# Kernel optimization log

Measured on AMD Instinct MI355X. Metric: run time of the kernel, lower is better.

Reference implementation:

```python
import jax, jax.numpy as jnp
import numpy as np

EPS = 1e-5

def _layer_norm(x, g, b):
    mu = jnp.mean(x, axis=-1, keepdims=True)
    var = jnp.var(x, axis=-1, keepdims=True)
    return (x - mu) * jax.lax.rsqrt(var + EPS) * g + b

def setup_inputs() -> dict:
    key = jax.random.key(0)
    ks = jax.random.split(key, 20)
    B, S, D, L = 64, 1024, 16, 2
    s = 1.0 / np.sqrt(D)
    s2 = 1.0 / np.sqrt(L)
    return {
        "x": jax.random.normal(ks[0], (B, S, D), jnp.float32),
        "Wq": jax.random.uniform(ks[1], (D, L), jnp.float32, -s, s),
        "bq": jax.random.uniform(ks[2], (L,), jnp.float32, -s, s),
        "Wk": jax.random.uniform(ks[3], (D, L), jnp.float32, -s, s),
        "bk": jax.random.uniform(ks[4], (L,), jnp.float32, -s, s),
        "Wv": jax.random.uniform(ks[5], (D, L), jnp.float32, -s, s),
        "bv": jax.random.uniform(ks[6], (L,), jnp.float32, -s, s),
        "Wu": jax.random.uniform(ks[7], (L, D), jnp.float32, -s2, s2),
        "bu": jax.random.uniform(ks[8], (D,), jnp.float32, -s2, s2),
        "ln_g": jnp.ones((D,), jnp.float32),
        "ln_b": jnp.zeros((D,), jnp.float32),
        "W1": jax.random.uniform(ks[9], (D, D), jnp.float32, -s, s),
        "b1": jax.random.uniform(ks[10], (D,), jnp.float32, -s, s),
        "W2": jax.random.uniform(ks[11], (D, D), jnp.float32, -s, s),
        "b2": jax.random.uniform(ks[12], (D,), jnp.float32, -s, s),
        "W3": jax.random.uniform(ks[13], (D, D), jnp.float32, -s, s),
        "b3": jax.random.uniform(ks[14], (D,), jnp.float32, -s, s),
        "Wo": jax.random.uniform(ks[15], (D, D), jnp.float32, -s, s),
        "bo": jax.random.uniform(ks[16], (D,), jnp.float32, -s, s),
    }

def reference(x, Wq, bq, Wk, bk, Wv, bv, Wu, bu, ln_g, ln_b, W1, b1, W2, b2, W3, b3, Wo, bo):
    D = 16  # embedding_dim used as softmax scale in the original
    Q = x @ Wq + bq                      # [B,S,2]
    K = x @ Wk + bk
    V = x @ Wv + bv
    scores = jnp.einsum('bsl,btl->bst', Q, K) / jnp.sqrt(jnp.float32(D))  # [B,S,S]
    attn = jax.nn.softmax(scores, axis=-1)
    ctx = jnp.einsum('bst,btl->bsl', attn, V)  # [B,S,2]
    ctx = ctx @ Wu + bu                         # [B,S,16]
    h = _layer_norm(ctx + x, ln_g, ln_b)
    ff = ((h @ W1 + b1) @ W2 + b2) @ W3 + b3   # 3 linears, no nonlinearity (as in source)
    out = _layer_norm(ff + h, ln_g, ln_b)       # NOTE: same LayerNorm params reused, per source
    return out @ Wo + bo
```

## Files before the change

### kernel.cpp

```cpp
#include <hip/hip_runtime.h>
#include <math.h>


__device__ __forceinline__ void load_row16(const float* __restrict__ p, float* dst) {
    const float4* p4 = (const float4*)p;
    float4 r0 = p4[0], r1 = p4[1], r2 = p4[2], r3 = p4[3];
    dst[0]=r0.x;  dst[1]=r0.y;  dst[2]=r0.z;  dst[3]=r0.w;
    dst[4]=r1.x;  dst[5]=r1.y;  dst[6]=r1.z;  dst[7]=r1.w;
    dst[8]=r2.x;  dst[9]=r2.y;  dst[10]=r2.z; dst[11]=r2.w;
    dst[12]=r3.x; dst[13]=r3.y; dst[14]=r3.z; dst[15]=r3.w;
}

__device__ __forceinline__ void matvec16(const float* v, const float* W,
                                         const float* __restrict__ bias, float* y) {
#pragma unroll
    for (int j = 0; j < 16; ++j) y[j] = bias[j];
#pragma unroll
    for (int i = 0; i < 16; ++i) {
        float vi = v[i];
#pragma unroll
        for (int j = 0; j < 16; ++j) y[j] = fmaf(vi, W[i*16 + j], y[j]);
    }
}

__device__ __forceinline__ void layernorm16(float* h, const float* __restrict__ g,
                                            const float* __restrict__ bb) {
    float mu = 0.f;
#pragma unroll
    for (int j = 0; j < 16; ++j) mu += h[j];
    mu *= 0.0625f;
    float var = 0.f;
#pragma unroll
    for (int j = 0; j < 16; ++j) { float d = h[j] - mu; var = fmaf(d, d, var); }
    var *= 0.0625f;
    float rs = rsqrtf(var + 1e-5f);
#pragma unroll
    for (int j = 0; j < 16; ++j) h[j] = (h[j] - mu) * rs * g[j] + bb[j];
}

__global__ __launch_bounds__(1024)
void fused_encoder(const float* __restrict__ x,
                   const float* __restrict__ Wq, const float* __restrict__ bq,
                   const float* __restrict__ Wk, const float* __restrict__ bk,
                   const float* __restrict__ Wv, const float* __restrict__ bv,
                   const float* __restrict__ Wu, const float* __restrict__ bu,
                   const float* __restrict__ ln_g, const float* __restrict__ ln_b,
                   const float* __restrict__ W1, const float* __restrict__ b1,
                   const float* __restrict__ W2, const float* __restrict__ b2,
                   const float* __restrict__ W3, const float* __restrict__ b3,
                   const float* __restrict__ Wo, const float* __restrict__ bo,
                   float* __restrict__ out)
{
    constexpr int S = 1024, D = 16;

    __shared__ float4 skv[1024];
    __shared__ float4 sred[3][256];
    __shared__ float  sW[4][256];

    const int tid     = threadIdx.x;
    const int b       = blockIdx.x >> 2;
    const int chunk   = blockIdx.x & 3;
    const int q_local = tid & 255;
    const int kslice  = tid >> 8;

    const float* xb = x + (size_t)b * S * D;

    {
        float xr[16];
        load_row16(xb + tid * D, xr);
        float k0 = bk[0], k1 = bk[1], v0 = bv[0], v1 = bv[1];
#pragma unroll
        for (int i = 0; i < 16; ++i) {
            k0 = fmaf(xr[i], Wk[2*i],   k0);
            k1 = fmaf(xr[i], Wk[2*i+1], k1);
            v0 = fmaf(xr[i], Wv[2*i],   v0);
            v1 = fmaf(xr[i], Wv[2*i+1], v1);
        }
        skv[tid] = make_float4(k0, k1, v0, v1);
    }

    {
        const float* Wsel = (kslice == 0) ? W1 : (kslice == 1) ? W2
                          : (kslice == 2) ? W3 : Wo;
        sW[kslice][q_local] = Wsel[q_local];
    }

    const int qi = chunk * 256 + q_local;
    float xq[16];
    load_row16(xb + qi * D, xq);
    float q0 = bq[0], q1 = bq[1];
#pragma unroll
    for (int i = 0; i < 16; ++i) {
        q0 = fmaf(xq[i], Wq[2*i],   q0);
        q1 = fmaf(xq[i], Wq[2*i+1], q1);
    }
    q0 *= 0.25f; q1 *= 0.25f;

    __syncthreads();

    float l0=0.f, l1=0.f, l2=0.f, l3=0.f;
    float a00=0.f, a01=0.f, a02=0.f, a03=0.f;
    float a10=0.f, a11=0.f, a12=0.f, a13=0.f;
    const int t0 = kslice * 256;
    for (int t = 0; t < 256; t += 4) {
        float4 c0 = skv[t0 + t + 0];
        float4 c1 = skv[t0 + t + 1];
        float4 c2 = skv[t0 + t + 2];
        float4 c3 = skv[t0 + t + 3];
        float p0 = __expf(fmaf(q1, c0.y, q0 * c0.x));
        float p1 = __expf(fmaf(q1, c1.y, q0 * c1.x));
        float p2 = __expf(fmaf(q1, c2.y, q0 * c2.x));
        float p3 = __expf(fmaf(q1, c3.y, q0 * c3.x));
        l0 += p0; a00 = fmaf(p0, c0.z, a00); a10 = fmaf(p0, c0.w, a10);
        l1 += p1; a01 = fmaf(p1, c1.z, a01); a11 = fmaf(p1, c1.w, a11);
        l2 += p2; a02 = fmaf(p2, c2.z, a02); a12 = fmaf(p2, c2.w, a12);
        l3 += p3; a03 = fmaf(p3, c3.z, a03); a13 = fmaf(p3, c3.w, a13);
    }
    float l  = (l0 + l1) + (l2 + l3);
    float a0 = (a00 + a01) + (a02 + a03);
    float a1 = (a10 + a11) + (a12 + a13);

    if (kslice > 0) sred[kslice - 1][q_local] = make_float4(l, a0, a1, 0.f);
    __syncthreads();

    if (tid < 256) {
#pragma unroll
        for (int s = 0; s < 3; ++s) {
            float4 r = sred[s][tid];
            l += r.x; a0 += r.y; a1 += r.z;
        }
        float rl = 1.0f / l;
        float c0 = a0 * rl, c1 = a1 * rl;

        float h[16];
#pragma unroll
        for (int j = 0; j < 16; ++j)
            h[j] = fmaf(c0, Wu[j], fmaf(c1, Wu[16 + j], bu[j])) + xq[j];

        layernorm16(h, ln_g, ln_b);

        float t1[16], t2[16], t3[16];
        matvec16(h,  &sW[0][0], b1, t1);
        matvec16(t1, &sW[1][0], b2, t2);
        matvec16(t2, &sW[2][0], b3, t3);
#pragma unroll
        for (int j = 0; j < 16; ++j) t3[j] += h[j];

        layernorm16(t3, ln_g, ln_b);

        float o[16];
        matvec16(t3, &sW[3][0], bo, o);

        float4* orow = (float4*)(out + ((size_t)b * S + qi) * D);
        orow[0] = make_float4(o[0],  o[1],  o[2],  o[3]);
        orow[1] = make_float4(o[4],  o[5],  o[6],  o[7]);
        orow[2] = make_float4(o[8],  o[9],  o[10], o[11]);
        orow[3] = make_float4(o[12], o[13], o[14], o[15]);
    }
}

extern "C" void kernel_launch(void* const* d_in, const int* in_sizes, int n_in,
                              void* d_out, int out_size, void* d_ws, size_t ws_size,
                              hipStream_t stream) {
    const float* x    = (const float*)d_in[0];
    const float* Wq   = (const float*)d_in[1];
    const float* bq   = (const float*)d_in[2];
    const float* Wk   = (const float*)d_in[3];
    const float* bk   = (const float*)d_in[4];
    const float* Wv   = (const float*)d_in[5];
    const float* bv   = (const float*)d_in[6];
    const float* Wu   = (const float*)d_in[7];
    const float* bu   = (const float*)d_in[8];
    const float* ln_g = (const float*)d_in[9];
    const float* ln_b = (const float*)d_in[10];
    const float* W1   = (const float*)d_in[11];
    const float* b1   = (const float*)d_in[12];
    const float* W2   = (const float*)d_in[13];
    const float* b2   = (const float*)d_in[14];
    const float* W3   = (const float*)d_in[15];
    const float* b3   = (const float*)d_in[16];
    const float* Wo   = (const float*)d_in[17];
    const float* bo   = (const float*)d_in[18];
    float* out = (float*)d_out;

    dim3 grid(256), block(1024);
    hipLaunchKernelGGL(fused_encoder, grid, block, 0, stream,
                       x, Wq, bq, Wk, bk, Wv, bv, Wu, bu, ln_g, ln_b,
                       W1, b1, W2, b2, W3, b3, Wo, bo, out);
}
```

Baseline: 114.2 us.

## Split K/V projection into separate kernel and read KV from global memory

K/V projection moves into its own kernel that writes a float4 KV buffer to workspace, with the softmax scale folded into K. The attention kernel then uses 512 blocks of 512 threads and streams KV through global/cached loads with a wave-uniform base pointer, instead of projecting all 1024 keys per block into shared memory. This removes the fourfold redundant K/V projection and the large LDS tile, and doubles the block count. The cost is an extra launch, a global round trip for KV, and cache-served rather than LDS loads in the inner loop.

```diff
diff --git a/kernel.cpp b/kernel.cpp
--- a/kernel.cpp
+++ b/kernel.cpp
@@ -38,11 +38,29 @@
     for (int j = 0; j < 16; ++j) h[j] = (h[j] - mu) * rs * g[j] + bb[j];
 }
 
-__global__ __launch_bounds__(1024)
-void fused_encoder(const float* __restrict__ x,
+__global__ __launch_bounds__(256)
+void kv_proj(const float* __restrict__ x,
+             const float* __restrict__ Wk, const float* __restrict__ bk,
+             const float* __restrict__ Wv, const float* __restrict__ bv,
+             float4* __restrict__ kv)
+{
+    const int r = blockIdx.x * 256 + threadIdx.x;
+    float xr[16];
+    load_row16(x + (size_t)r * 16, xr);
+    float k0 = bk[0], k1 = bk[1], v0 = bv[0], v1 = bv[1];
+#pragma unroll
+    for (int i = 0; i < 16; ++i) {
+        k0 = fmaf(xr[i], Wk[2*i],   k0);
+        k1 = fmaf(xr[i], Wk[2*i+1], k1);
+        v0 = fmaf(xr[i], Wv[2*i],   v0);
+        v1 = fmaf(xr[i], Wv[2*i+1], v1);
+    }
+    kv[r] = make_float4(k0 * 0.25f, k1 * 0.25f, v0, v1);
+}
+
+__global__ __launch_bounds__(512)
+void attn_epilogue(const float* __restrict__ x, const float4* __restrict__ kv,
                    const float* __restrict__ Wq, const float* __restrict__ bq,
-                   const float* __restrict__ Wk, const float* __restrict__ bk,
-                   const float* __restrict__ Wv, const float* __restrict__ bv,
                    const float* __restrict__ Wu, const float* __restrict__ bu,
                    const float* __restrict__ ln_g, const float* __restrict__ ln_b,
                    const float* __restrict__ W1, const float* __restrict__ b1,
@@ -51,79 +69,54 @@
                    const float* __restrict__ Wo, const float* __restrict__ bo,
                    float* __restrict__ out)
 {
-    constexpr int S = 1024, D = 16;
-
-    __shared__ float4 skv[1024];
-    __shared__ float4 sred[3][256];
+    __shared__ float4 sred[3][128];
     __shared__ float  sW[4][256];
 
     const int tid     = threadIdx.x;
-    const int b       = blockIdx.x >> 2;
-    const int chunk   = blockIdx.x & 3;
-    const int q_local = tid & 255;
-    const int kslice  = tid >> 8;
-
-    const float* xb = x + (size_t)b * S * D;
+    const int b       = blockIdx.x >> 3;
+    const int chunk   = blockIdx.x & 7;
+    const int q_local = tid & 127;
+    const int kslice  = tid >> 7;
 
     {
-        float xr[16];
-        load_row16(xb + tid * D, xr);
-        float k0 = bk[0], k1 = bk[1], v0 = bv[0], v1 = bv[1];
-#pragma unroll
-        for (int i = 0; i < 16; ++i) {
-            k0 = fmaf(xr[i], Wk[2*i],   k0);
-            k1 = fmaf(xr[i], Wk[2*i+1], k1);
-            v0 = fmaf(xr[i], Wv[2*i],   v0);
-            v1 = fmaf(xr[i], Wv[2*i+1], v1);
-        }
-        skv[tid] = make_float4(k0, k1, v0, v1);
+        float* sWf = &sW[0][0];
+        sWf[tid]       = (tid < 256) ? W1[tid] : W2[tid - 256];
+        const int j = tid + 512;
+        sWf[j]         = (j < 768) ? W3[j - 512] : Wo[j - 768];
     }
 
-    {
-        const float* Wsel = (kslice == 0) ? W1 : (kslice == 1) ? W2
-                          : (kslice == 2) ? W3 : Wo;
-        sW[kslice][q_local] = Wsel[q_local];
-    }
-
-    const int qi = chunk * 256 + q_local;
+    const int qi = chunk * 128 + q_local;
+    const float* xb = x + (size_t)b * 1024 * 16;
     float xq[16];
-    load_row16(xb + qi * D, xq);
+    load_row16(xb + qi * 16, xq);
     float q0 = bq[0], q1 = bq[1];
 #pragma unroll
     for (int i = 0; i < 16; ++i) {
         q0 = fmaf(xq[i], Wq[2*i],   q0);
         q1 = fmaf(xq[i], Wq[2*i+1], q1);
     }
-    q0 *= 0.25f; q1 *= 0.25f;
 
-    __syncthreads();
+    const int ks = __builtin_amdgcn_readfirstlane(kslice);
+    const float4* __restrict__ kvp = kv + ((size_t)b << 10) + (ks << 8);
 
-    float l0=0.f, l1=0.f, l2=0.f, l3=0.f;
-    float a00=0.f, a01=0.f, a02=0.f, a03=0.f;
-    float a10=0.f, a11=0.f, a12=0.f, a13=0.f;
-    const int t0 = kslice * 256;
-    for (int t = 0; t < 256; t += 4) {
-        float4 c0 = skv[t0 + t + 0];
-        float4 c1 = skv[t0 + t + 1];
-        float4 c2 = skv[t0 + t + 2];
-        float4 c3 = skv[t0 + t + 3];
+    float l0=0.f, l1=0.f, a00=0.f, a01=0.f, a10=0.f, a11=0.f;
+#pragma unroll 4
+    for (int t = 0; t < 256; t += 2) {
+        const float4 c0 = kvp[t];
+        const float4 c1 = kvp[t + 1];
         float p0 = __expf(fmaf(q1, c0.y, q0 * c0.x));
         float p1 = __expf(fmaf(q1, c1.y, q0 * c1.x));
-        float p2 = __expf(fmaf(q1, c2.y, q0 * c2.x));
-        float p3 = __expf(fmaf(q1, c3.y, q0 * c3.x));
         l0 += p0; a00 = fmaf(p0, c0.z, a00); a10 = fmaf(p0, c0.w, a10);
         l1 += p1; a01 = fmaf(p1, c1.z, a01); a11 = fmaf(p1, c1.w, a11);
-        l2 += p2; a02 = fmaf(p2, c2.z, a02); a12 = fmaf(p2, c2.w, a12);
-        l3 += p3; a03 = fmaf(p3, c3.z, a03); a13 = fmaf(p3, c3.w, a13);
     }
-    float l  = (l0 + l1) + (l2 + l3);
-    float a0 = (a00 + a01) + (a02 + a03);
-    float a1 = (a10 + a11) + (a12 + a13);
+    float l  = l0 + l1;
+    float a0 = a00 + a01;
+    float a1 = a10 + a11;
 
     if (kslice > 0) sred[kslice - 1][q_local] = make_float4(l, a0, a1, 0.f);
     __syncthreads();
 
-    if (tid < 256) {
+    if (tid < 128) {
 #pragma unroll
         for (int s = 0; s < 3; ++s) {
             float4 r = sred[s][tid];
@@ -151,7 +144,7 @@
         float o[16];
         matvec16(t3, &sW[3][0], bo, o);
 
-        float4* orow = (float4*)(out + ((size_t)b * S + qi) * D);
+        float4* orow = (float4*)(out + ((size_t)b * 1024 + qi) * 16);
         orow[0] = make_float4(o[0],  o[1],  o[2],  o[3]);
         orow[1] = make_float4(o[4],  o[5],  o[6],  o[7]);
         orow[2] = make_float4(o[8],  o[9],  o[10], o[11]);
@@ -182,9 +175,11 @@
     const float* Wo   = (const float*)d_in[17];
     const float* bo   = (const float*)d_in[18];
     float* out = (float*)d_out;
+    float4* kvws = (float4*)d_ws;
 
-    dim3 grid(256), block(1024);
-    hipLaunchKernelGGL(fused_encoder, grid, block, 0, stream,
-                       x, Wq, bq, Wk, bk, Wv, bv, Wu, bu, ln_g, ln_b,
+    hipLaunchKernelGGL(kv_proj, dim3(256), dim3(256), 0, stream,
+                       x, Wk, bk, Wv, bv, kvws);
+    hipLaunchKernelGGL(attn_epilogue, dim3(512), dim3(512), 0, stream,
+                       x, kvws, Wq, bq, Wu, bu, ln_g, ln_b,
                        W1, b1, W2, b2, W3, b3, Wo, bo, out);
 }
```

After: 128.5 us. 1.13x slower.

## Register-tile four queries per thread over 16 key slices with exp2 softmax

Applied to the files above, without the earlier changes.

Each thread now handles four queries against a 64-key slice instead of one query against a 256-key slice, so every K/V float4 read from shared memory is reused for four queries. The softmax scale is folded with log2(e) so the hardware exp2 instruction replaces __expf. Partial sums from 16 slices are reduced through larger shared arrays. This cuts LDS traffic per exp, at the cost of more shared memory, a 16-way reduction, and higher register pressure.

```diff
diff --git a/kernel.cpp b/kernel.cpp
--- a/kernel.cpp
+++ b/kernel.cpp
@@ -51,23 +51,24 @@
                    const float* __restrict__ Wo, const float* __restrict__ bo,
                    float* __restrict__ out)
 {
-    constexpr int S = 1024, D = 16;
-
     __shared__ float4 skv[1024];
-    __shared__ float4 sred[3][256];
-    __shared__ float  sW[4][256];
-
-    const int tid     = threadIdx.x;
-    const int b       = blockIdx.x >> 2;
-    const int chunk   = blockIdx.x & 3;
-    const int q_local = tid & 255;
-    const int kslice  = tid >> 8;
-
-    const float* xb = x + (size_t)b * S * D;
+    __shared__ float2 sq[256];
+    __shared__ float  sW[1024];
+    __shared__ float  sl [16][256];
+    __shared__ float  sa0[16][256];
+    __shared__ float  sa1[16][256];
+
+    const int tid  = threadIdx.x;
+    const int b    = blockIdx.x >> 2;
+    const int chunk= blockIdx.x & 3;
+    const int lane = tid & 63;
+    const int ks   = tid >> 6;
+
+    const float* xb = x + (size_t)b * 1024 * 16;
 
     {
         float xr[16];
-        load_row16(xb + tid * D, xr);
+        load_row16(xb + tid * 16, xr);
         float k0 = bk[0], k1 = bk[1], v0 = bv[0], v1 = bv[1];
 #pragma unroll
         for (int i = 0; i < 16; ++i) {
@@ -80,57 +81,68 @@
     }
 
     {
-        const float* Wsel = (kslice == 0) ? W1 : (kslice == 1) ? W2
-                          : (kslice == 2) ? W3 : Wo;
-        sW[kslice][q_local] = Wsel[q_local];
-    }
-
-    const int qi = chunk * 256 + q_local;
-    float xq[16];
-    load_row16(xb + qi * D, xq);
-    float q0 = bq[0], q1 = bq[1];
-#pragma unroll
-    for (int i = 0; i < 16; ++i) {
-        q0 = fmaf(xq[i], Wq[2*i],   q0);
-        q1 = fmaf(xq[i], Wq[2*i+1], q1);
-    }
-    q0 *= 0.25f; q1 *= 0.25f;
-
+        const float* Ws = (tid < 256) ? W1 : (tid < 512) ? W2
+                        : (tid < 768) ? W3 : Wo;
+        sW[tid] = Ws[tid & 255];
+    }
+
+    if (tid < 256) {
+        const int qi = chunk * 256 + tid;
+        float xr[16];
+        load_row16(xb + qi * 16, xr);
+        float q0 = bq[0], q1 = bq[1];
+#pragma unroll
+        for (int i = 0; i < 16; ++i) {
+            q0 = fmaf(xr[i], Wq[2*i],   q0);
+            q1 = fmaf(xr[i], Wq[2*i+1], q1);
+        }
+        const float SC = 0.25f * 1.44269504088896340736f;
+        sq[tid] = make_float2(q0 * SC, q1 * SC);
+    }
     __syncthreads();
 
-    float l0=0.f, l1=0.f, l2=0.f, l3=0.f;
-    float a00=0.f, a01=0.f, a02=0.f, a03=0.f;
-    float a10=0.f, a11=0.f, a12=0.f, a13=0.f;
-    const int t0 = kslice * 256;
-    for (int t = 0; t < 256; t += 4) {
-        float4 c0 = skv[t0 + t + 0];
-        float4 c1 = skv[t0 + t + 1];
-        float4 c2 = skv[t0 + t + 2];
-        float4 c3 = skv[t0 + t + 3];
-        float p0 = __expf(fmaf(q1, c0.y, q0 * c0.x));
-        float p1 = __expf(fmaf(q1, c1.y, q0 * c1.x));
-        float p2 = __expf(fmaf(q1, c2.y, q0 * c2.x));
-        float p3 = __expf(fmaf(q1, c3.y, q0 * c3.x));
-        l0 += p0; a00 = fmaf(p0, c0.z, a00); a10 = fmaf(p0, c0.w, a10);
-        l1 += p1; a01 = fmaf(p1, c1.z, a01); a11 = fmaf(p1, c1.w, a11);
-        l2 += p2; a02 = fmaf(p2, c2.z, a02); a12 = fmaf(p2, c2.w, a12);
-        l3 += p3; a03 = fmaf(p3, c3.z, a03); a13 = fmaf(p3, c3.w, a13);
-    }
-    float l  = (l0 + l1) + (l2 + l3);
-    float a0 = (a00 + a01) + (a02 + a03);
-    float a1 = (a10 + a11) + (a12 + a13);
-
-    if (kslice > 0) sred[kslice - 1][q_local] = make_float4(l, a0, a1, 0.f);
+    float q0[4], q1[4], L[4], A0[4], A1[4];
+#pragma unroll
+    for (int j = 0; j < 4; ++j) {
+        float2 qq = sq[lane + 64*j];
+        q0[j] = qq.x; q1[j] = qq.y;
+        L[j] = 0.f; A0[j] = 0.f; A1[j] = 0.f;
+    }
+    const int kbase = ks * 64;
+    for (int t = 0; t < 64; t += 2) {
+        const float4 c0 = skv[kbase + t];
+        const float4 c1 = skv[kbase + t + 1];
+#pragma unroll
+        for (int j = 0; j < 4; ++j) {
+            float p0 = __builtin_amdgcn_exp2f(fmaf(q1[j], c0.y, q0[j] * c0.x));
+            float p1 = __builtin_amdgcn_exp2f(fmaf(q1[j], c1.y, q0[j] * c1.x));
+            L[j] += p0;  A0[j] = fmaf(p0, c0.z, A0[j]);  A1[j] = fmaf(p0, c0.w, A1[j]);
+            L[j] += p1;  A0[j] = fmaf(p1, c1.z, A0[j]);  A1[j] = fmaf(p1, c1.w, A1[j]);
+        }
+    }
+#pragma unroll
+    for (int j = 0; j < 4; ++j) {
+        const int q = lane + 64*j;
+        sl [ks][q] = L[j];
+        sa0[ks][q] = A0[j];
+        sa1[ks][q] = A1[j];
+    }
     __syncthreads();
 
     if (tid < 256) {
-#pragma unroll
-        for (int s = 0; s < 3; ++s) {
-            float4 r = sred[s][tid];
-            l += r.x; a0 += r.y; a1 += r.z;
-        }
-        float rl = 1.0f / l;
-        float c0 = a0 * rl, c1 = a1 * rl;
+        float l = 0.f, a0 = 0.f, a1 = 0.f;
+#pragma unroll
+        for (int s = 0; s < 16; ++s) {
+            l  += sl [s][tid];
+            a0 += sa0[s][tid];
+            a1 += sa1[s][tid];
+        }
+        const float rl = 1.0f / l;
+        const float c0 = a0 * rl, c1 = a1 * rl;
+
+        const int qi = chunk * 256 + tid;
+        float xq[16];
+        load_row16(xb + qi * 16, xq);
 
         float h[16];
 #pragma unroll
@@ -140,18 +152,18 @@
         layernorm16(h, ln_g, ln_b);
 
         float t1[16], t2[16], t3[16];
-        matvec16(h,  &sW[0][0], b1, t1);
-        matvec16(t1, &sW[1][0], b2, t2);
-        matvec16(t2, &sW[2][0], b3, t3);
+        matvec16(h,  sW,       b1, t1);
+        matvec16(t1, sW + 256, b2, t2);
+        matvec16(t2, sW + 512, b3, t3);
 #pragma unroll
         for (int j = 0; j < 16; ++j) t3[j] += h[j];
 
         layernorm16(t3, ln_g, ln_b);
 
         float o[16];
-        matvec16(t3, &sW[3][0], bo, o);
-
-        float4* orow = (float4*)(out + ((size_t)b * S + qi) * D);
+        matvec16(t3, sW + 768, bo, o);
+
+        float4* orow = (float4*)(out + ((size_t)b * 1024 + qi) * 16);
         orow[0] = make_float4(o[0],  o[1],  o[2],  o[3]);
         orow[1] = make_float4(o[4],  o[5],  o[6],  o[7]);
         orow[2] = make_float4(o[8],  o[9],  o[10], o[11]);
@@ -183,8 +195,7 @@
     const float* bo   = (const float*)d_in[18];
     float* out = (float*)d_out;
 
-    dim3 grid(256), block(1024);
-    hipLaunchKernelGGL(fused_encoder, grid, block, 0, stream,
+    hipLaunchKernelGGL(fused_encoder, dim3(256), dim3(1024), 0, stream,
                        x, Wq, bq, Wk, bk, Wv, bv, Wu, bu, ln_g, ln_b,
                        W1, b1, W2, b2, W3, b3, Wo, bo, out);
 }
```

Result: no change. 112.8 us (-1.3%).
